# Performance work log

Measured on AMD Instinct MI355X. Metric: run time of the kernel, lower is better.

## Reference

```python
import jax, jax.numpy as jnp
import numpy as np
from jax import lax

DIM = 256
HEADS = 8
DIM_HEAD = 32
INNER = HEADS * DIM_HEAD  # 256
SCALE = DIM_HEAD ** -0.5
EPS = 1e-5
DN = ('NCHW', 'OIHW', 'NCHW')


def chan_layer_norm(x, g):
    # LayerNorm over channel dim (axis=1), biased variance
    mean = jnp.mean(x, axis=1, keepdims=True)
    var = jnp.mean((x - mean) ** 2, axis=1, keepdims=True)
    return (x - mean) / jnp.sqrt(var + EPS) * g


def conv1x1(x, w):
    return lax.conv_general_dilated(x, w, (1, 1), 'VALID', dimension_numbers=DN)


def dwconv3x3(x, w):
    # depthwise 3x3, padding=1, groups=channels; w: [C,1,3,3]
    return lax.conv_general_dilated(x, w, (1, 1), 'SAME', dimension_numbers=DN,
                                    feature_group_count=x.shape[1])


def setup_inputs() -> dict:
    key = jax.random.key(0)
    ks = jax.random.split(key, 9)
    B, X, Y = 16, 64, 64
    fmap = jax.random.normal(ks[0], (B, DIM, X, Y), dtype=jnp.float32)
    w = lambda k, shape: (jax.random.normal(k, shape, dtype=jnp.float32) * 0.02)
    return {
        'fmap': fmap,
        'g_norm': jnp.ones((1, DIM, 1, 1), dtype=jnp.float32),
        'wq1': w(ks[1], (INNER, DIM, 1, 1)),
        'wq_dw': w(ks[2], (INNER, 1, 3, 3)),
        'wk1': w(ks[3], (INNER, DIM, 1, 1)),
        'wk_dw': w(ks[4], (INNER, 1, 3, 3)),
        'wv1': w(ks[5], (INNER, DIM, 1, 1)),
        'wv_dw': w(ks[6], (INNER, 1, 3, 3)),
        'wo': w(ks[7], (DIM, INNER, 1, 1)),
        'g_out': jnp.ones((1, DIM, 1, 1), dtype=jnp.float32),
    }


def reference(fmap, g_norm, wq1, wq_dw, wk1, wk_dw, wv1, wv_dw, wo, g_out):
    b, _, X, Y = fmap.shape
    n = X * Y
    x = chan_layer_norm(fmap, g_norm)
    # QKV: 1x1 conv -> depthwise 3x3 conv (dropout is identity in eval)
    q = dwconv3x3(conv1x1(x, wq1), wq_dw)
    k = dwconv3x3(conv1x1(x, wk1), wk_dw)
    v = dwconv3x3(conv1x1(x, wv1), wv_dw)
    # b (h c) x y -> b h n c
    def split(t):
        return t.reshape(b, HEADS, DIM_HEAD, n).transpose(0, 1, 3, 2)
    q, k, v = split(q), split(k), split(v)
    q = jax.nn.softmax(q, axis=-1) * SCALE   # softmax over feature dim
    k = jax.nn.softmax(k, axis=-2)           # softmax over sequence dim
    ctx = jnp.einsum('bhnd,bhne->bhde', k, v)    # [b,h,d,d]
    out = jnp.einsum('bhnd,bhde->bhne', q, ctx)  # [b,h,n,d]
    # b h n d -> b (h d) x y
    out = out.transpose(0, 1, 3, 2).reshape(b, INNER, X, Y)
    out = jax.nn.silu(out)
    out = conv1x1(out, wo)
    return chan_layer_norm(out, g_out)
```

## Files before the change

kernel.cpp:

```cpp
#include <hip/hip_runtime.h>


typedef unsigned short u16;
typedef __bf16 bf16x8 __attribute__((ext_vector_type(8)));
typedef float f32x4 __attribute__((ext_vector_type(4)));
typedef float f32x16 __attribute__((ext_vector_type(16)));

#define DEV static __device__ __forceinline__

DEV float b2f(u16 u) { return __uint_as_float(((unsigned int)u) << 16); }
DEV u16 f2bf(float f) {
  unsigned int u = __float_as_uint(f);
  return (u16)((u + 0x7fffu + ((u >> 16) & 1u)) >> 16);
}
DEV void gl2lds16(const void* g, void* l) {
  __builtin_amdgcn_global_load_lds((__attribute__((address_space(1))) void*)g,
                                   (__attribute__((address_space(3))) void*)l, 16, 0, 0);
}

__global__ __launch_bounds__(256) void prep_kernel(const float* __restrict__ wk,
                                                   const float* __restrict__ wv,
                                                   const float* __restrict__ wq,
                                                   const float* __restrict__ wo,
                                                   u16* __restrict__ wb) {
  const int i = blockIdx.x * 256 + threadIdx.x;
  const int yb = blockIdx.y;
  if (yb == 0)      wb[(i >> 8) * 512 + (i & 255)] = f2bf(wk[i]);
  else if (yb == 1) wb[(i >> 8) * 512 + 256 + (i & 255)] = f2bf(wv[i]);
  else if (yb == 2) wb[131072 + i] = f2bf(wq[i]);
  else              wb[196608 + i] = f2bf(wo[i]);
}

__global__ __launch_bounds__(256) void ln_tin_kernel(const float* __restrict__ f,
                                                     const float* __restrict__ g,
                                                     u16* __restrict__ xT) {
  __shared__ u16 tile[64 * 258];
  __shared__ float red[2 * 256];
  __shared__ float mu_s[64], inv_s[64];
  const int t = threadIdx.x;
  const int p0 = blockIdx.x * 64;
  const int b = blockIdx.y;
  const long fb = (long)b * 256 * 4096;
  const int p = t & 63, cg = t >> 6;
  float s1 = 0.f, s2 = 0.f;
  for (int pass = 0; pass < 64; ++pass) {
    int c = pass * 4 + cg;
    float v = f[fb + (long)c * 4096 + p0 + p];
    s1 += v; s2 += v * v;
    tile[p * 258 + c] = f2bf(v);
  }
  red[cg * 64 + p] = s1;
  red[256 + cg * 64 + p] = s2;
  __syncthreads();
  if (t < 64) {
    float a1 = red[t] + red[64 + t] + red[128 + t] + red[192 + t];
    float a2 = red[256 + t] + red[320 + t] + red[384 + t] + red[448 + t];
    float mu = a1 * (1.f / 256.f);
    float var = a2 * (1.f / 256.f) - mu * mu;
    mu_s[t] = mu;
    inv_s[t] = 1.0f / sqrtf(var + 1e-5f);
  }
  __syncthreads();
  {
    float gc = g[t];
    for (int pp = 0; pp < 64; ++pp) {
      float v = b2f(tile[pp * 258 + t]);
      xT[((long)b * 4096 + p0 + pp) * 256 + t] = f2bf((v - mu_s[pp]) * inv_s[pp] * gc);
    }
  }
}

__global__ __launch_bounds__(256) void gemm_bt_kernel(
    const u16* __restrict__ A, const u16* __restrict__ B0, const u16* __restrict__ B1,
    u16* __restrict__ Cg, int ldc, long sA, long sC) {
  __shared__ u16 As[128 * 32];
  __shared__ u16 Bs[128 * 32];
  const int t = threadIdx.x;
  const int wave = t >> 6, lane = t & 63, quad = lane >> 4, l16 = lane & 15;
  const int wr = wave >> 1, wc = wave & 1;
  const int m0 = blockIdx.x * 128;
  const int jt = blockIdx.y;
  const int b = blockIdx.z;
  const u16* Ab = A + (long)b * sA + (long)m0 * 256;
  const u16* Bt = (jt < 2 ? B0 : B1) + (jt & 1) * 128 * 256;
  u16* Cb = Cg + (long)b * sC + (long)m0 * ldc + jt * 128;

  const int srow = lane >> 2;
  const int scol = (lane & 3) * 8;
  f32x4 acc[4][4];
#pragma unroll
  for (int i = 0; i < 4; ++i)
#pragma unroll
    for (int j = 0; j < 4; ++j) acc[i][j] = (f32x4){0.f, 0.f, 0.f, 0.f};

  const int aoff = (wr * 64 + l16) * 32 + quad * 8;
  const int boff = (wc * 64 + l16) * 32 + quad * 8;

  for (int ks = 0; ks < 8; ++ks) {
    const int k0 = ks * 32;
    __syncthreads();
    for (int i = wave; i < 8; i += 4) {
      gl2lds16(Ab + (i * 16 + srow) * 256 + k0 + scol, &As[i * 512 + lane * 8]);
      gl2lds16(Bt + (i * 16 + srow) * 256 + k0 + scol, &Bs[i * 512 + lane * 8]);
    }
    __syncthreads();
    bf16x8 af[4], bfr[4];
#pragma unroll
    for (int mt = 0; mt < 4; ++mt) af[mt] = *(const bf16x8*)&As[aoff + mt * 512];
#pragma unroll
    for (int nt = 0; nt < 4; ++nt) bfr[nt] = *(const bf16x8*)&Bs[boff + nt * 512];
#pragma unroll
    for (int mt = 0; mt < 4; ++mt)
#pragma unroll
      for (int nt = 0; nt < 4; ++nt)
        acc[mt][nt] = __builtin_amdgcn_mfma_f32_16x16x32_bf16(af[mt], bfr[nt], acc[mt][nt], 0, 0, 0);
  }
#pragma unroll
  for (int mt = 0; mt < 4; ++mt) {
    const int mbase = wr * 64 + mt * 16 + quad * 4;
#pragma unroll
    for (int nt = 0; nt < 4; ++nt) {
      const int n = wc * 64 + nt * 16 + l16;
#pragma unroll
      for (int r = 0; r < 4; ++r)
        Cb[(long)(mbase + r) * ldc + n] = f2bf(acc[mt][nt][r]);
    }
  }
}

__global__ __launch_bounds__(256) void dwq_kernel(const u16* __restrict__ qT,
                                                  const float* __restrict__ wdw,
                                                  u16* __restrict__ qp) {
  __shared__ u16 tile[6 * 66 * 40];
  const int t = threadIdx.x;
  const int strip = blockIdx.x, h = blockIdx.y, b = blockIdx.z;
  const int x0 = strip * 4;
  const int wave = t >> 6, lane = t & 63;
  const int ysel = lane & 15, cg = lane >> 4;
  const int y = wave * 16 + ysel;
  const int ty = t >> 2, tc = t & 3;

  if (t < 48) {
    const int slot = t >> 3, brd = (t >> 2) & 1, c4 = t & 3;
    *(uint4*)&tile[slot * 2640 + (brd ? 65 * 40 : 0) + c4 * 8] = (uint4){0, 0, 0, 0};
  }
  const u16* qrow = qT + (long)b * 4096 * 256 + h * 32 + tc * 8;
#pragma unroll
  for (int s = 0; s < 6; ++s) {
    const int xx = x0 - 1 + s;
    uint4 v = (uint4){0, 0, 0, 0};
    if ((unsigned)xx < 64u) v = *(const uint4*)(qrow + (long)(xx * 64 + ty) * 256);
    *(uint4*)&tile[s * 2640 + (ty + 1) * 40 + tc * 8] = v;
  }
  float w[72];
#pragma unroll
  for (int q = 0; q < 8; ++q)
#pragma unroll
    for (int i = 0; i < 9; ++i) w[q * 9 + i] = wdw[(h * 32 + cg * 8 + q) * 9 + i];
  __syncthreads();

  u16* ob = qp + ((long)b * 4096 + y) * 256 + h * 32 + cg * 8;
#pragma unroll
  for (int it = 0; it < 4; ++it) {
    const int x = x0 + it;
    float acc[8] = {0.f, 0.f, 0.f, 0.f, 0.f, 0.f, 0.f, 0.f};
#pragma unroll
    for (int r = 0; r < 3; ++r) {
#pragma unroll
      for (int dy = 0; dy < 3; ++dy) {
        uint4 pk = *(const uint4*)&tile[(it + r) * 2640 + (y + dy) * 40 + cg * 8];
        const u16* s = (const u16*)&pk;
#pragma unroll
        for (int q = 0; q < 8; ++q)
          acc[q] = fmaf(w[q * 9 + r * 3 + dy], b2f(s[q]), acc[q]);
      }
    }
    float e[8];
    float s = 0.f;
#pragma unroll
    for (int q = 0; q < 8; ++q) { e[q] = __expf(acc[q]); s += e[q]; }
    s += __shfl_xor(s, 16);
    s += __shfl_xor(s, 32);
    const float inv = 0.17677669529663687f / s;
    uint4 o;
    u16* os = (u16*)&o;
#pragma unroll
    for (int q = 0; q < 8; ++q) os[q] = f2bf(e[q] * inv);
    *(uint4*)(ob + (long)x * 16384) = o;
  }
}

__global__ __launch_bounds__(1024, 4) void ctx_kernel(const u16* __restrict__ kvT,
                                                      const float* __restrict__ wkdw,
                                                      const float* __restrict__ wvdw,
                                                      float* __restrict__ par0,
                                                      float* __restrict__ par1) {
  __shared__ float redb[8 * 1088];
  __shared__ float redk[16 * 32];
  const int t = threadIdx.x;
  const int strip = blockIdx.x, h = blockIdx.y, b = blockIdx.z;
  const int wave = t >> 6, lane = t & 63;
  const int g = wave >> 2, wq = wave & 3;
  const int x0 = strip * 32 + g * 8;
  const int c = lane & 31, half = lane >> 5;
  const int ystart = wq * 16 + half * 8;
  float wk[9], wv[9];
#pragma unroll
  for (int i = 0; i < 9; ++i) {
    wk[i] = wkdw[(h * 32 + c) * 9 + i];
    wv[i] = wvdw[(h * 32 + c) * 9 + i];
  }
  const u16* kb = kvT + (long)b * 4096 * 512 + 2 * (h * 32 + c);

  float fk[3][10], fv[3][10];
  unsigned pk[10];
#pragma unroll
  for (int r = 0; r < 2; ++r) {
    const int x = x0 - 1 + r;
#pragma unroll
    for (int m = 0; m < 10; ++m) {
      const int yy = ystart - 1 + m;
      float a = 0.f, bb = 0.f;
      if (((unsigned)x < 64u) & ((unsigned)yy < 64u)) {
        const unsigned u = *(const unsigned*)(kb + (long)(x * 64 + yy) * 512);
        a = b2f((u16)(u & 0xffffu));
        bb = b2f((u16)(u >> 16));
      }
      fk[r][m] = a; fv[r][m] = bb;
    }
  }
#pragma unroll
  for (int m = 0; m < 10; ++m) {
    const int yy = ystart - 1 + m;
    unsigned u = 0;
    if (((unsigned)(x0 + 1) < 64u) & ((unsigned)yy < 64u))
      u = *(const unsigned*)(kb + (long)((x0 + 1) * 64 + yy) * 512);
    pk[m] = u;
  }
#pragma unroll
  for (int m = 0; m < 10; ++m) {
    fk[2][m] = __uint_as_float(pk[m] << 16);
    fv[2][m] = __uint_as_float(pk[m] & 0xffff0000u);
  }
  f32x16 acc;
#pragma unroll
  for (int r = 0; r < 16; ++r) acc[r] = 0.f;
  float ks = 0.f;

  for (int it = 0; it < 8; ++it) {
    const int xn = x0 + it + 2;
#pragma unroll
    for (int m = 0; m < 10; ++m) {
      const int yy = ystart - 1 + m;
      unsigned u = 0;
      if (((unsigned)xn < 64u) & ((unsigned)yy < 64u))
        u = *(const unsigned*)(kb + (long)(xn * 64 + yy) * 512);
      pk[m] = u;
    }
    union { bf16x8 v; u16 s[8]; } af, bf_;
#pragma unroll
    for (int j = 0; j < 8; ++j) {
      float a = 0.f, bb = 0.f;
#pragma unroll
      for (int r = 0; r < 3; ++r)
#pragma unroll
        for (int dy = 0; dy < 3; ++dy) {
          a = fmaf(wk[r * 3 + dy], fk[r][j + dy], a);
          bb = fmaf(wv[r * 3 + dy], fv[r][j + dy], bb);
        }
      const u16 eb = f2bf(__expf(a));
      ks += b2f(eb);
      af.s[j] = eb;
      bf_.s[j] = f2bf(bb);
    }
    acc = __builtin_amdgcn_mfma_f32_32x32x16_bf16(af.v, bf_.v, acc, 0, 0, 0);
#pragma unroll
    for (int m = 0; m < 10; ++m) {
      fk[0][m] = fk[1][m]; fv[0][m] = fv[1][m];
      fk[1][m] = fk[2][m]; fv[1][m] = fv[2][m];
      fk[2][m] = __uint_as_float(pk[m] << 16);
      fv[2][m] = __uint_as_float(pk[m] & 0xffff0000u);
    }
  }
  ks += __shfl_xor(ks, 32);
  if (half == 0) redk[wave * 32 + c] = ks;
  if (wave >= 8) {
#pragma unroll
    for (int r = 0; r < 16; ++r) redb[(wave - 8) * 1088 + lane * 17 + r] = acc[r];
  }
  __syncthreads();
  if (wave < 8) {
#pragma unroll
    for (int r = 0; r < 16; ++r) acc[r] += redb[wave * 1088 + lane * 17 + r];
  }
  __syncthreads();
  if (wave >= 4 && wave < 8) {
#pragma unroll
    for (int r = 0; r < 16; ++r) redb[(wave - 4) * 1088 + lane * 17 + r] = acc[r];
  }
  __syncthreads();
  if (wave < 4) {
#pragma unroll
    for (int r = 0; r < 16; ++r) acc[r] += redb[wave * 1088 + lane * 17 + r];
  }
  __syncthreads();
  if (wave >= 1 && wave < 4) {
#pragma unroll
    for (int r = 0; r < 16; ++r) redb[(wave - 1) * 1088 + lane * 17 + r] = acc[r];
  }
  __syncthreads();
  if (wave == 0) {
    float* par = (strip ? par1 : par0) + (long)(b * 8 + h) * 1056;
#pragma unroll
    for (int r = 0; r < 16; ++r) {
      float sum = acc[r] + redb[lane * 17 + r] + redb[1088 + lane * 17 + r] +
                  redb[2176 + lane * 17 + r];
      const int d = (r & 3) + 8 * (r >> 2) + 4 * half;
      par[d * 32 + c] = sum;
    }
    if (t < 32) {
      float s = 0.f;
#pragma unroll
      for (int w = 0; w < 16; ++w) s += redk[w * 32 + t];
      par[1024 + t] = s;
    }
  }
}

__global__ __launch_bounds__(256) void reduce_kernel(const float* __restrict__ par0,
                                                     const float* __restrict__ par1,
                                                     float* __restrict__ ctxF,
                                                     float* __restrict__ ksF) {
  const int bh = blockIdx.x;
  const long base = (long)bh * 1056;
  for (int i = threadIdx.x; i < 1056; i += 256) {
    float v = par0[base + i] + par1[base + i];
    if (i < 1024) ctxF[(long)bh * 1024 + i] = v;
    else ksF[(long)bh * 32 + (i - 1024)] = v;
  }
}

__global__ __launch_bounds__(256) void attn_kernel(const u16* __restrict__ qp,
                                                   const float* __restrict__ ctxg,
                                                   const float* __restrict__ ksumg,
                                                   u16* __restrict__ sout) {
  __shared__ u16 cnhi[2 * 32 * 40];
  __shared__ u16 cnlo[2 * 32 * 40];
  const int t = threadIdx.x;
  const int p0 = blockIdx.x * 128;
  const int hp = blockIdx.y;
  const int b = blockIdx.z;
  const int wave = t >> 6, lane = t & 63, quad = lane >> 4, l16 = lane & 15;

  for (int j = 0; j < 8; ++j) {
    const int lidx = j * 256 + t;
    const int e = lidx & 31, d = (lidx >> 5) & 31, hh = lidx >> 10;
    const int gd = (hp * 2 + hh) * 32 + d;
    const float c = ctxg[(long)b * 8192 + gd * 32 + e] / ksumg[(long)b * 256 + gd];
    const u16 hi = f2bf(c);
    cnhi[hh * 1280 + e * 40 + d] = hi;
    cnlo[hh * 1280 + e * 40 + d] = f2bf(c - b2f(hi));
  }
  __syncthreads();

  const u16* qb = qp + ((long)b * 4096 + p0 + wave * 32) * 256;
  u16* ob = sout + ((long)b * 4096 + p0 + wave * 32) * 256;
#pragma unroll
  for (int hh = 0; hh < 2; ++hh) {
    const int h = hp * 2 + hh;
    const int cb = hh * 1280 + quad * 8;
    const bf16x8 bhi0 = *(const bf16x8*)&cnhi[cb + l16 * 40];
    const bf16x8 bhi1 = *(const bf16x8*)&cnhi[cb + (16 + l16) * 40];
    const bf16x8 blo0 = *(const bf16x8*)&cnlo[cb + l16 * 40];
    const bf16x8 blo1 = *(const bf16x8*)&cnlo[cb + (16 + l16) * 40];
#pragma unroll
    for (int rt = 0; rt < 2; ++rt) {
      const bf16x8 af = *(const bf16x8*)&qb[(rt * 16 + l16) * 256 + h * 32 + quad * 8];
      f32x4 a0 = (f32x4){0.f, 0.f, 0.f, 0.f};
      f32x4 a1 = (f32x4){0.f, 0.f, 0.f, 0.f};
      a0 = __builtin_amdgcn_mfma_f32_16x16x32_bf16(af, blo0, a0, 0, 0, 0);
      a0 = __builtin_amdgcn_mfma_f32_16x16x32_bf16(af, bhi0, a0, 0, 0, 0);
      a1 = __builtin_amdgcn_mfma_f32_16x16x32_bf16(af, blo1, a1, 0, 0, 0);
      a1 = __builtin_amdgcn_mfma_f32_16x16x32_bf16(af, bhi1, a1, 0, 0, 0);
#pragma unroll
      for (int r = 0; r < 4; ++r) {
        const int row = rt * 16 + quad * 4 + r;
        const float v0 = a0[r], v1 = a1[r];
        ob[(long)row * 256 + h * 32 + l16] = f2bf(v0 / (1.f + __expf(-v0)));
        ob[(long)row * 256 + h * 32 + 16 + l16] = f2bf(v1 / (1.f + __expf(-v1)));
      }
    }
  }
}

__global__ __launch_bounds__(256) void ln_tout_kernel(const u16* __restrict__ y,
                                                      const float* __restrict__ gout,
                                                      float* __restrict__ out) {
  __shared__ u16 tile[64 * 258];
  __shared__ float red[2 * 256];
  __shared__ float mu_s[64], inv_s[64];
  const int t = threadIdx.x;
  const int p0 = blockIdx.x * 64;
  const int b = blockIdx.y;
  for (int p = 0; p < 64; ++p)
    tile[p * 258 + t] = y[((long)b * 4096 + p0 + p) * 256 + t];
  __syncthreads();
  {
    const int p = t & 63, part = t >> 6;
    float s1 = 0.f, s2 = 0.f;
    for (int k = 0; k < 64; ++k) {
      float v = b2f(tile[p * 258 + part * 64 + k]);
      s1 += v; s2 += v * v;
    }
    red[part * 64 + p] = s1;
    red[256 + part * 64 + p] = s2;
  }
  __syncthreads();
  if (t < 64) {
    float s1 = red[t] + red[64 + t] + red[128 + t] + red[192 + t];
    float s2 = red[256 + t] + red[320 + t] + red[384 + t] + red[448 + t];
    float mu = s1 * (1.f / 256.f);
    float var = s2 * (1.f / 256.f) - mu * mu;
    mu_s[t] = mu;
    inv_s[t] = 1.0f / sqrtf(var + 1e-5f);
  }
  __syncthreads();
  {
    const int p = t & 63, cg = t >> 6;
    const long ob = (long)b * 256 * 4096;
    for (int pass = 0; pass < 64; ++pass) {
      int c = pass * 4 + cg;
      float v = b2f(tile[p * 258 + c]);
      out[ob + (long)c * 4096 + p0 + p] = (v - mu_s[p]) * inv_s[p] * gout[c];
    }
  }
}

extern "C" void kernel_launch(void* const* d_in, const int* in_sizes, int n_in,
                              void* d_out, int out_size, void* d_ws, size_t ws_size,
                              hipStream_t stream) {
  (void)in_sizes; (void)n_in; (void)out_size; (void)ws_size;
  const float* fmap = (const float*)d_in[0];
  const float* gnorm = (const float*)d_in[1];
  const float* wq1 = (const float*)d_in[2];
  const float* wqdw = (const float*)d_in[3];
  const float* wk1 = (const float*)d_in[4];
  const float* wkdw = (const float*)d_in[5];
  const float* wv1 = (const float*)d_in[6];
  const float* wvdw = (const float*)d_in[7];
  const float* wo = (const float*)d_in[8];
  const float* gout = (const float*)d_in[9];
  float* out = (float*)d_out;
  char* ws = (char*)d_ws;

  float* par0 = (float*)(ws);
  u16* wb = (u16*)(ws + 540672);
  float* par1 = (float*)(ws + 1064960);
  u16* wkv_bf = wb;
  u16* wq_bf = wb + 131072;
  u16* wo_bf = wb + 196608;
  u16* xT = (u16*)(ws + 2097152);
  u16* kvT = (u16*)(ws + 35651584);
  u16* qT = kvT;
  float* ctxF = (float*)(ws + 35651584);
  float* ksF = (float*)(ws + 35651584 + 524288);
  u16* qp = (u16*)(ws + 69206016);
  u16* sbuf = xT;
  u16* ybuf = qp;

  prep_kernel<<<dim3(256, 4), 256, 0, stream>>>(wk1, wv1, wq1, wo, wb);
  ln_tin_kernel<<<dim3(64, 16), 256, 0, stream>>>(fmap, gnorm, xT);
  gemm_bt_kernel<<<dim3(32, 4, 16), 256, 0, stream>>>(xT, wkv_bf, wkv_bf + 65536, kvT, 512,
                                                      4096L * 256, 4096L * 512);
  ctx_kernel<<<dim3(2, 8, 16), 1024, 0, stream>>>(kvT, wkdw, wvdw, par0, par1);
  gemm_bt_kernel<<<dim3(32, 2, 16), 256, 0, stream>>>(xT, wq_bf, wq_bf, qT, 256,
                                                      4096L * 256, 4096L * 256);
  dwq_kernel<<<dim3(16, 8, 16), 256, 0, stream>>>(qT, wqdw, qp);
  reduce_kernel<<<dim3(128), 256, 0, stream>>>(par0, par1, ctxF, ksF);
  attn_kernel<<<dim3(32, 4, 16), 256, 0, stream>>>(qp, ctxF, ksF, sbuf);
  gemm_bt_kernel<<<dim3(32, 2, 16), 256, 0, stream>>>(sbuf, wo_bf, wo_bf, ybuf, 256,
                                                      4096L * 256, 4096L * 256);
  ln_tout_kernel<<<dim3(64, 16), 256, 0, stream>>>(ybuf, gout, out);
}
```

Before: 311.8 us.

## Vectorize layernorm transpose kernels and fold partial-context reduction into attention

The input layernorm now writes xT with 16-byte vector stores, and the output layernorm reads y with 16-byte vector loads straight from global memory, fusing the statistics pass with the LDS fill. The LDS row stride changes from 258 to 268 to allow aligned vector LDS access. The separate reduce kernel is removed: attn_kernel sums par0 and par1 itself, which saves one launch but repeats that small reduction in every attention block.

Result: faster. 304.2 us (-2.5%).

```diff
diff --git a/kernel.cpp b/kernel.cpp
--- a/kernel.cpp
+++ b/kernel.cpp
@@ -34,7 +34,7 @@
 __global__ __launch_bounds__(256) void ln_tin_kernel(const float* __restrict__ f,
                                                      const float* __restrict__ g,
                                                      u16* __restrict__ xT) {
-  __shared__ u16 tile[64 * 258];
+  __shared__ u16 tile[64 * 268];
   __shared__ float red[2 * 256];
   __shared__ float mu_s[64], inv_s[64];
   const int t = threadIdx.x;
@@ -47,7 +47,7 @@
     int c = pass * 4 + cg;
     float v = f[fb + (long)c * 4096 + p0 + p];
     s1 += v; s2 += v * v;
-    tile[p * 258 + c] = f2bf(v);
+    tile[p * 268 + c] = f2bf(v);
   }
   red[cg * 64 + p] = s1;
   red[256 + cg * 64 + p] = s2;
@@ -62,10 +62,25 @@
   }
   __syncthreads();
   {
-    float gc = g[t];
-    for (int pp = 0; pp < 64; ++pp) {
-      float v = b2f(tile[pp * 258 + t]);
-      xT[((long)b * 4096 + p0 + pp) * 256 + t] = f2bf((v - mu_s[pp]) * inv_s[pp] * gc);
+    const int ch8 = (t & 31) * 8, wp = t >> 5;
+    float ga[8];
+#pragma unroll
+    for (int e = 0; e < 8; ++e) ga[e] = g[ch8 + e];
+#pragma unroll
+    for (int pass = 0; pass < 8; ++pass) {
+      const int px = pass * 8 + wp;
+      uint2 lo = *(const uint2*)&tile[px * 268 + ch8];
+      uint2 hi = *(const uint2*)&tile[px * 268 + ch8 + 4];
+      const u16* sl = (const u16*)&lo;
+      const u16* sh = (const u16*)&hi;
+      const float mu = mu_s[px], inv = inv_s[px];
+      uint4 o;
+      u16* os = (u16*)&o;
+#pragma unroll
+      for (int e = 0; e < 4; ++e) os[e] = f2bf((b2f(sl[e]) - mu) * inv * ga[e]);
+#pragma unroll
+      for (int e = 0; e < 4; ++e) os[4 + e] = f2bf((b2f(sh[e]) - mu) * inv * ga[4 + e]);
+      *(uint4*)&xT[((long)b * 4096 + p0 + px) * 256 + ch8] = o;
     }
   }
 }
@@ -327,22 +342,9 @@
   }
 }
 
-__global__ __launch_bounds__(256) void reduce_kernel(const float* __restrict__ par0,
-                                                     const float* __restrict__ par1,
-                                                     float* __restrict__ ctxF,
-                                                     float* __restrict__ ksF) {
-  const int bh = blockIdx.x;
-  const long base = (long)bh * 1056;
-  for (int i = threadIdx.x; i < 1056; i += 256) {
-    float v = par0[base + i] + par1[base + i];
-    if (i < 1024) ctxF[(long)bh * 1024 + i] = v;
-    else ksF[(long)bh * 32 + (i - 1024)] = v;
-  }
-}
-
 __global__ __launch_bounds__(256) void attn_kernel(const u16* __restrict__ qp,
-                                                   const float* __restrict__ ctxg,
-                                                   const float* __restrict__ ksumg,
+                                                   const float* __restrict__ par0,
+                                                   const float* __restrict__ par1,
                                                    u16* __restrict__ sout) {
   __shared__ u16 cnhi[2 * 32 * 40];
   __shared__ u16 cnlo[2 * 32 * 40];
@@ -355,8 +357,9 @@
   for (int j = 0; j < 8; ++j) {
     const int lidx = j * 256 + t;
     const int e = lidx & 31, d = (lidx >> 5) & 31, hh = lidx >> 10;
-    const int gd = (hp * 2 + hh) * 32 + d;
-    const float c = ctxg[(long)b * 8192 + gd * 32 + e] / ksumg[(long)b * 256 + gd];
+    const long base = (long)(b * 8 + hp * 2 + hh) * 1056;
+    const float ks = par0[base + 1024 + d] + par1[base + 1024 + d];
+    const float c = (par0[base + d * 32 + e] + par1[base + d * 32 + e]) / ks;
     const u16 hi = f2bf(c);
     cnhi[hh * 1280 + e * 40 + d] = hi;
     cnlo[hh * 1280 + e * 40 + d] = f2bf(c - b2f(hi));
@@ -396,24 +399,31 @@
 __global__ __launch_bounds__(256) void ln_tout_kernel(const u16* __restrict__ y,
                                                       const float* __restrict__ gout,
                                                       float* __restrict__ out) {
-  __shared__ u16 tile[64 * 258];
+  __shared__ u16 tile[64 * 268];
   __shared__ float red[2 * 256];
   __shared__ float mu_s[64], inv_s[64];
   const int t = threadIdx.x;
   const int p0 = blockIdx.x * 64;
   const int b = blockIdx.y;
-  for (int p = 0; p < 64; ++p)
-    tile[p * 258 + t] = y[((long)b * 4096 + p0 + p) * 256 + t];
-  __syncthreads();
   {
-    const int p = t & 63, part = t >> 6;
+    const int px = t >> 2, q = t & 3;
+    const u16* yrow = y + ((long)b * 4096 + p0 + px) * 256;
     float s1 = 0.f, s2 = 0.f;
-    for (int k = 0; k < 64; ++k) {
-      float v = b2f(tile[p * 258 + part * 64 + k]);
-      s1 += v; s2 += v * v;
-    }
-    red[part * 64 + p] = s1;
-    red[256 + part * 64 + p] = s2;
+#pragma unroll
+    for (int j = 0; j < 8; ++j) {
+      const int ch = q * 8 + j * 32;
+      uint4 v = *(const uint4*)&yrow[ch];
+      const u16* s = (const u16*)&v;
+#pragma unroll
+      for (int e = 0; e < 8; ++e) {
+        float fv = b2f(s[e]);
+        s1 += fv; s2 += fv * fv;
+      }
+      *(uint2*)&tile[px * 268 + ch] = (uint2){v.x, v.y};
+      *(uint2*)&tile[px * 268 + ch + 4] = (uint2){v.z, v.w};
+    }
+    red[q * 64 + px] = s1;
+    red[256 + q * 64 + px] = s2;
   }
   __syncthreads();
   if (t < 64) {
@@ -426,12 +436,17 @@
   }
   __syncthreads();
   {
-    const int p = t & 63, cg = t >> 6;
+    const int lpx = t & 63, cw = t >> 6;
     const long ob = (long)b * 256 * 4096;
-    for (int pass = 0; pass < 64; ++pass) {
-      int c = pass * 4 + cg;
-      float v = b2f(tile[p * 258 + c]);
-      out[ob + (long)c * 4096 + p0 + p] = (v - mu_s[p]) * inv_s[p] * gout[c];
+    const float mu = mu_s[lpx], inv = inv_s[lpx];
+#pragma unroll
+    for (int pass = 0; pass < 16; ++pass) {
+      const int c4 = pass * 16 + cw * 4;
+      uint2 v = *(const uint2*)&tile[lpx * 268 + c4];
+      const u16* s = (const u16*)&v;
+#pragma unroll
+      for (int i = 0; i < 4; ++i)
+        out[ob + (long)(c4 + i) * 4096 + p0 + lpx] = (b2f(s[i]) - mu) * inv * gout[c4 + i];
     }
   }
 }
@@ -462,8 +477,6 @@
   u16* xT = (u16*)(ws + 2097152);
   u16* kvT = (u16*)(ws + 35651584);
   u16* qT = kvT;
-  float* ctxF = (float*)(ws + 35651584);
-  float* ksF = (float*)(ws + 35651584 + 524288);
   u16* qp = (u16*)(ws + 69206016);
   u16* sbuf = xT;
   u16* ybuf = qp;
@@ -476,8 +489,7 @@
   gemm_bt_kernel<<<dim3(32, 2, 16), 256, 0, stream>>>(xT, wq_bf, wq_bf, qT, 256,
                                                       4096L * 256, 4096L * 256);
   dwq_kernel<<<dim3(16, 8, 16), 256, 0, stream>>>(qT, wqdw, qp);
-  reduce_kernel<<<dim3(128), 256, 0, stream>>>(par0, par1, ctxF, ksF);
-  attn_kernel<<<dim3(32, 4, 16), 256, 0, stream>>>(qp, ctxF, ksF, sbuf);
+  attn_kernel<<<dim3(32, 4, 16), 256, 0, stream>>>(qp, par0, par1, sbuf);
   gemm_bt_kernel<<<dim3(32, 2, 16), 256, 0, stream>>>(sbuf, wo_bf, wo_bf, ybuf, 256,
                                                       4096L * 256, 4096L * 256);
   ln_tout_kernel<<<dim3(64, 16), 256, 0, stream>>>(ybuf, gout, out);
```
